# Optimization experiments

Measured on AMD Instinct MI355X. Metric: run time of the kernel, lower is better.

The kernel has to match this reference:

```python
import jax, jax.numpy as jnp
import numpy as np

N_NODES = 20000
N_EDGES = 320000
F_IN = 256
HID = 256
N_CLS = 5


def _glorot(key, shape):
    lim = np.sqrt(6.0 / (shape[0] + shape[1]))
    return jax.random.uniform(key, shape, jnp.float32, -lim, lim)


def setup_inputs() -> dict:
    key = jax.random.key(0)
    ks = jax.random.split(key, 12)
    x1 = jax.random.normal(ks[0], (N_NODES, F_IN), jnp.float32)
    x2 = jax.random.normal(ks[1], (N_NODES, F_IN), jnp.float32)
    ei1 = jax.random.randint(ks[2], (2, N_EDGES), 0, N_NODES, jnp.int64 if jax.config.jax_enable_x64 else jnp.int32)
    ei2 = jax.random.randint(ks[3], (2, N_EDGES), 0, N_NODES, jnp.int64 if jax.config.jax_enable_x64 else jnp.int32)
    params = {
        'W1': _glorot(ks[4], (F_IN, HID)), 'b1': jnp.zeros((HID,), jnp.float32),
        'W2': _glorot(ks[5], (HID, HID)), 'b2': jnp.zeros((HID,), jnp.float32),
        'W3': _glorot(ks[6], (HID, HID)), 'b3': jnp.zeros((HID,), jnp.float32),
        'Wl': _glorot(ks[7], (HID, N_CLS)), 'bl': jnp.zeros((N_CLS,), jnp.float32),
    }
    return {'x1': x1, 'edge_index1': ei1, 'x2': x2, 'edge_index2': ei2, **params}


def gcn_conv(x, edge_index, W, b):
    # PyG GCNConv: add self-loops, symmetric normalization D^-1/2 (A+I) D^-1/2 (X W) + b
    N = x.shape[0]
    src, dst = edge_index[0], edge_index[1]
    deg = jax.ops.segment_sum(jnp.ones(src.shape[0], x.dtype), dst, num_segments=N) + 1.0
    dinv = jax.lax.rsqrt(deg)  # [N]
    xw = x @ W                 # [N, H]
    coef = (dinv[src] * dinv[dst])[:, None]  # per-edge norm
    agg = jax.ops.segment_sum(xw[src] * coef, dst, num_segments=N)
    agg = agg + xw * (dinv * dinv)[:, None]  # self-loop term
    return agg + b


def _branch(x, ei, W1, b1, W2, b2, W3, b3):
    # dropout is identity in eval mode
    h = jax.nn.relu(gcn_conv(x, ei, W1, b1))
    h = jax.nn.relu(gcn_conv(h, ei, W2, b2))
    return gcn_conv(h, ei, W3, b3)


def reference(x1, edge_index1, x2, edge_index2, W1, b1, W2, b2, W3, b3, Wl, bl):
    h1 = _branch(x1, edge_index1, W1, b1, W2, b2, W3, b3)
    h2 = _branch(x2, edge_index2, W1, b1, W2, b2, W3, b3)
    h = jnp.concatenate([h1, h2], axis=0)          # [2N, H]
    pooled = jnp.mean(h, axis=0, keepdims=True)    # batch is all zeros -> single mean pool
    return pooled @ Wl + bl                        # [1, num_classes]
```

## Files before the change

### kernel.cpp

```cpp
#include <hip/hip_runtime.h>
#include <hip/hip_bf16.h>

#define N_NODES 20000
#define N_EDGES 320000
#define HID 256

typedef __attribute__((ext_vector_type(8))) short bf16x8;
typedef __attribute__((ext_vector_type(4))) float f32x4;

__device__ __forceinline__ float bf2f(ushort u) {
  union { unsigned int i; float f; } v; v.i = ((unsigned int)u) << 16; return v.f;
}
__device__ __forceinline__ ushort f2bf(float f) {
  union { float f; unsigned int i; } v; v.f = f;
  unsigned int r = v.i + 0x7FFFu + ((v.i >> 16) & 1u);
  return (ushort)(r >> 16);
}

__global__ void detect_kernel(const void* x1, const void* ei1, int* flags) {
  __shared__ int cnt_wild, cnt_oddnz;
  if (threadIdx.x == 0) { cnt_wild = 0; cnt_oddnz = 0; }
  __syncthreads();
  const ushort* xu = (const ushort*)x1;
  int wild = 0;
#pragma unroll
  for (int k = 0; k < 4; k++) {
    ushort u = xu[threadIdx.x * 4 + k];
    int ex = (u >> 7) & 0xFF;
    if (ex >= 0x90) wild++;
  }
  if (wild) atomicAdd(&cnt_wild, wild);
  const int* ii = (const int*)ei1;
  if (ii[threadIdx.x * 2 + 1] != 0) atomicAdd(&cnt_oddnz, 1);
  __syncthreads();
  if (threadIdx.x == 0) {
    flags[0] = (cnt_wild > 64) ? 1 : 0;
    flags[1] = (cnt_oddnz < 8) ? 1 : 0;
  }
}

__global__ void init_kernel(int* cnt0, int* cnt1, float* t0, float* t1) {
  int i = blockIdx.x * blockDim.x + threadIdx.x;
  if (i < N_NODES) { cnt0[i] = 0; cnt1[i] = 0; t0[i] = 0.f; t1[i] = 0.f; }
}

__global__ void cvt_ei_count_kernel(const void* e0, const void* e1,
                                    int* o0, int* o1,
                                    int* cnt0, int* cnt1,
                                    int* rank0, int* rank1, const int* flags) {
  int b = blockIdx.y;
  const void* e = b ? e1 : e0;
  int* o = b ? o1 : o0;
  int* cnt = b ? cnt1 : cnt0;
  int* rank = b ? rank1 : rank0;
  int i = blockIdx.x * 256 + threadIdx.x;
  if (i >= 2 * N_EDGES) return;
  int v = flags[1] ? (int)((const long long*)e)[i] : ((const int*)e)[i];
  o[i] = v;
  if (i >= N_EDGES) rank[i - N_EDGES] = atomicAdd(&cnt[v], 1);
}

__global__ void cvt_x_kernel(const void* x0, const void* x1v,
                             ushort* o0, ushort* o1, const int* flags) {
  const void* x = blockIdx.y ? x1v : x0;
  ushort* o = blockIdx.y ? o1 : o0;
  int i4 = (blockIdx.x * 256 + threadIdx.x) * 4;
  if (i4 >= N_NODES * HID) return;
  if (flags[0]) {
    float4 v = *(const float4*)((const float*)x + i4);
    ushort4 w; w.x = f2bf(v.x); w.y = f2bf(v.y); w.z = f2bf(v.z); w.w = f2bf(v.w);
    *(ushort4*)(o + i4) = w;
  } else {
    *(ushort4*)(o + i4) = *(const ushort4*)((const ushort*)x + i4);
  }
}

__global__ void cvt_w_kernel(const void* W1, const void* W2, const void* W3, const void* Wl,
                             const void* b1, const void* b2, const void* b3, const void* bl,
                             ushort* out, const int* flags) {
  int i = blockIdx.x * 256 + threadIdx.x;
  if (i >= 198661) return;
  const void* src; int off;
  if (i < 65536)       { src = W1; off = 0; }
  else if (i < 131072) { src = W2; off = 65536; }
  else if (i < 196608) { src = W3; off = 131072; }
  else if (i < 197888) { src = Wl; off = 196608; }
  else if (i < 198144) { src = b1; off = 197888; }
  else if (i < 198400) { src = b2; off = 198144; }
  else if (i < 198656) { src = b3; off = 198400; }
  else                 { src = bl; off = 198656; }
  int j = i - off;
  out[i] = flags[0] ? f2bf(((const float*)src)[j]) : ((const ushort*)src)[j];
}

__global__ __launch_bounds__(1024) void scan_kernel(const int* cnt0, const int* cnt1,
                                                    int* rp0, int* rp1,
                                                    float* dinv0, float* dinv1) {
  const int* cnt = blockIdx.x ? cnt1 : cnt0;
  int* rp = blockIdx.x ? rp1 : rp0;
  float* dinv = blockIdx.x ? dinv1 : dinv0;
  __shared__ int sd[1024];
  int tid = threadIdx.x;
  int base = tid * 20;
  int pref[20];
  int run = 0;
#pragma unroll
  for (int k = 0; k < 20; k++) {
    int i = base + k;
    int c = (i < N_NODES) ? cnt[i] : 0;
    if (i < N_NODES) dinv[i] = rsqrtf((float)c + 1.0f);
    run += c;
    pref[k] = run;
  }
  sd[tid] = run;
  __syncthreads();
  for (int off = 1; off < 1024; off <<= 1) {
    int v = (tid >= off) ? sd[tid - off] : 0;
    __syncthreads();
    sd[tid] += v;
    __syncthreads();
  }
  int offset = sd[tid] - run;
  if (tid == 0) rp[0] = 0;
#pragma unroll
  for (int k = 0; k < 20; k++) {
    int i = base + k;
    if (i < N_NODES) rp[i + 1] = offset + pref[k];
  }
}

__global__ void fill_kernel(const int* ei0, const int* ei1,
                            const float* dinv0, const float* dinv1,
                            const int* rp0, const int* rp1,
                            const int* rank0, const int* rank1,
                            int2* eg0, int2* eg1,
                            float* t0, float* t1) {
  int e = blockIdx.x * blockDim.x + threadIdx.x;
  if (e >= N_EDGES) return;
  int b = blockIdx.y;
  const int* ei = b ? ei1 : ei0;
  const float* dinv = b ? dinv1 : dinv0;
  const int* rp = b ? rp1 : rp0;
  const int* rank = b ? rank1 : rank0;
  int2* eg = b ? eg1 : eg0;
  float* t = b ? t1 : t0;
  int src = ei[e], dst = ei[N_EDGES + e];
  int slot = rp[dst] + rank[e];
  float dd = dinv[dst];
  eg[slot] = make_int2(src, __float_as_int(dinv[src] * dd));
  atomicAdd(&t[src], dd);
}

__global__ __launch_bounds__(256) void gemm_kernel(
    const ushort* __restrict__ A0, const ushort* __restrict__ A1,
    const ushort* __restrict__ W,
    ushort* __restrict__ C0, ushort* __restrict__ C1) {
  const ushort* A = blockIdx.z ? A1 : A0;
  ushort* C = blockIdx.z ? C1 : C0;
  int m0 = blockIdx.x * 64;
  int n0 = blockIdx.y * 64;
  __shared__ ushort As[64][40];
  __shared__ ushort Bs[64][40];
  int tid = threadIdx.x;
  int wave = tid >> 6, lane = tid & 63;
  int quad = lane >> 4, r16 = lane & 15;
  f32x4 acc0 = {0.f, 0.f, 0.f, 0.f}, acc1 = acc0, acc2 = acc0, acc3 = acc0;
  int la_row = tid >> 2;
  int la_off = (tid & 3) * 8;
  int lb_k = tid >> 3;
  int lb_n = (tid & 7) * 8;
  for (int k0 = 0; k0 < 256; k0 += 32) {
    int gr = m0 + la_row;
    int4 va = {0, 0, 0, 0};
    if (gr < N_NODES) va = *(const int4*)(A + gr * 256 + k0 + la_off);
    *(int4*)&As[la_row][la_off] = va;
    int4 vb = *(const int4*)(W + (k0 + lb_k) * 256 + n0 + lb_n);
    ushort tmp[8];
    *(int4*)tmp = vb;
#pragma unroll
    for (int j = 0; j < 8; j++) Bs[lb_n + j][lb_k] = tmp[j];
    __syncthreads();
    bf16x8 a  = *(const bf16x8*)&As[wave * 16 + r16][quad * 8];
    bf16x8 b0 = *(const bf16x8*)&Bs[r16][quad * 8];
    bf16x8 b1 = *(const bf16x8*)&Bs[16 + r16][quad * 8];
    bf16x8 b2 = *(const bf16x8*)&Bs[32 + r16][quad * 8];
    bf16x8 b3 = *(const bf16x8*)&Bs[48 + r16][quad * 8];
    acc0 = __builtin_amdgcn_mfma_f32_16x16x32_bf16(a, b0, acc0, 0, 0, 0);
    acc1 = __builtin_amdgcn_mfma_f32_16x16x32_bf16(a, b1, acc1, 0, 0, 0);
    acc2 = __builtin_amdgcn_mfma_f32_16x16x32_bf16(a, b2, acc2, 0, 0, 0);
    acc3 = __builtin_amdgcn_mfma_f32_16x16x32_bf16(a, b3, acc3, 0, 0, 0);
    __syncthreads();
  }
  int orow = m0 + wave * 16 + quad * 4;
#pragma unroll
  for (int r = 0; r < 4; r++) {
    int gr = orow + r;
    if (gr < N_NODES) {
      ushort* cp = C + gr * 256 + n0 + r16;
      cp[0]  = f2bf(acc0[r]);
      cp[16] = f2bf(acc1[r]);
      cp[32] = f2bf(acc2[r]);
      cp[48] = f2bf(acc3[r]);
    }
  }
}

__global__ __launch_bounds__(256) void agg_kernel(
    const ushort* __restrict__ XW0, const ushort* __restrict__ XW1,
    const float* __restrict__ dinv0, const float* __restrict__ dinv1,
    const int* __restrict__ rp0, const int* __restrict__ rp1,
    const int2* __restrict__ eg0, const int2* __restrict__ eg1,
    const ushort* __restrict__ bias,
    ushort* __restrict__ H0, ushort* __restrict__ H1) {
  int b = blockIdx.y;
  const ushort* XW = b ? XW1 : XW0;
  const float* dinv = b ? dinv1 : dinv0;
  const int* rp = b ? rp1 : rp0;
  const int2* eg = b ? eg1 : eg0;
  ushort* H = b ? H1 : H0;
  int wave = threadIdx.x >> 6, lane = threadIdx.x & 63;
  int i = blockIdx.x * 4 + wave;
  int f4 = lane * 4;
  float di = dinv[i];
  float self = di * di;
  ushort4 v = *(const ushort4*)(XW + i * 256 + f4);
  float a0 = self * bf2f(v.x), a1 = self * bf2f(v.y);
  float a2 = self * bf2f(v.z), a3 = self * bf2f(v.w);
  float c0_ = 0.f, c1_ = 0.f, c2_ = 0.f, c3_ = 0.f;
  int e0 = rp[i], e1 = rp[i + 1];
  int e = e0;
  for (; e + 3 < e1; e += 4) {
    int2 p0 = eg[e], p1 = eg[e + 1], p2 = eg[e + 2], p3 = eg[e + 3];
    ushort4 u0 = *(const ushort4*)(XW + p0.x * 256 + f4);
    ushort4 u1 = *(const ushort4*)(XW + p1.x * 256 + f4);
    ushort4 u2 = *(const ushort4*)(XW + p2.x * 256 + f4);
    ushort4 u3 = *(const ushort4*)(XW + p3.x * 256 + f4);
    float w0 = __int_as_float(p0.y), w1 = __int_as_float(p1.y);
    float w2 = __int_as_float(p2.y), w3 = __int_as_float(p3.y);
    a0 += w0 * bf2f(u0.x); a1 += w0 * bf2f(u0.y); a2 += w0 * bf2f(u0.z); a3 += w0 * bf2f(u0.w);
    c0_ += w1 * bf2f(u1.x); c1_ += w1 * bf2f(u1.y); c2_ += w1 * bf2f(u1.z); c3_ += w1 * bf2f(u1.w);
    a0 += w2 * bf2f(u2.x); a1 += w2 * bf2f(u2.y); a2 += w2 * bf2f(u2.z); a3 += w2 * bf2f(u2.w);
    c0_ += w3 * bf2f(u3.x); c1_ += w3 * bf2f(u3.y); c2_ += w3 * bf2f(u3.z); c3_ += w3 * bf2f(u3.w);
  }
  for (; e < e1; e++) {
    int2 pp = eg[e];
    float c = __int_as_float(pp.y);
    ushort4 u = *(const ushort4*)(XW + pp.x * 256 + f4);
    a0 += c * bf2f(u.x); a1 += c * bf2f(u.y); a2 += c * bf2f(u.z); a3 += c * bf2f(u.w);
  }
  a0 += c0_; a1 += c1_; a2 += c2_; a3 += c3_;
  ushort4 bb = *(const ushort4*)(bias + f4);
  a0 = fmaxf(a0 + bf2f(bb.x), 0.f);
  a1 = fmaxf(a1 + bf2f(bb.y), 0.f);
  a2 = fmaxf(a2 + bf2f(bb.z), 0.f);
  a3 = fmaxf(a3 + bf2f(bb.w), 0.f);
  ushort4 o; o.x = f2bf(a0); o.y = f2bf(a1); o.z = f2bf(a2); o.w = f2bf(a3);
  *(ushort4*)(H + i * 256 + f4) = o;
}

__global__ __launch_bounds__(256) void colsum_kernel(
    const ushort* __restrict__ H0, const ushort* __restrict__ H1,
    const float* __restrict__ dinv0, const float* __restrict__ dinv1,
    const float* __restrict__ t0, const float* __restrict__ t1,
    float* __restrict__ P) {
  int b = blockIdx.y;
  const ushort* H = b ? H1 : H0;
  const float* dinv = b ? dinv1 : dinv0;
  const float* t = b ? t1 : t0;
  int wave = threadIdx.x >> 6, lane = threadIdx.x & 63;
  int wid = blockIdx.x * 4 + wave;
  int f4 = lane * 4;
  float a0 = 0.f, a1 = 0.f, a2 = 0.f, a3 = 0.f;
  for (int j = wid; j < N_NODES; j += 256) {
    float dj = dinv[j];
    float c = dj * (t[j] + dj);
    ushort4 u = *(const ushort4*)(H + j * 256 + f4);
    a0 += c * bf2f(u.x); a1 += c * bf2f(u.y);
    a2 += c * bf2f(u.z); a3 += c * bf2f(u.w);
  }
  __shared__ float part[4][256];
  part[wave][f4 + 0] = a0; part[wave][f4 + 1] = a1;
  part[wave][f4 + 2] = a2; part[wave][f4 + 3] = a3;
  __syncthreads();
  int f = threadIdx.x;
  float ssum = part[0][f] + part[1][f] + part[2][f] + part[3][f];
  P[(b * 64 + blockIdx.x) * 256 + f] = ssum;
}

__global__ __launch_bounds__(256) void final_kernel(
    const float* __restrict__ P,
    const ushort* __restrict__ W3, const ushort* __restrict__ b3,
    const ushort* __restrict__ Wl, const ushort* __restrict__ bl,
    void* __restrict__ out, const int* __restrict__ flags) {
  __shared__ float v[256];
  __shared__ float pooled[256];
  int t = threadIdx.x;
  float acc0 = 0.f, acc1 = 0.f;
  for (int b = 0; b < 64; b++) {
    acc0 += P[b * 256 + t];
    acc1 += P[(64 + b) * 256 + t];
  }
  v[t] = acc0 + acc1;
  __syncthreads();
  float acc = 0.f;
  for (int f = 0; f < 256; f++) acc += v[f] * bf2f(W3[f * 256 + t]);
  pooled[t] = acc * (1.0f / (2.0f * N_NODES)) + bf2f(b3[t]);
  __syncthreads();
  if (t < 5) {
    float o = bf2f(bl[t]);
    for (int h = 0; h < 256; h++) o += pooled[h] * bf2f(Wl[h * 5 + t]);
    if (flags[0]) ((float*)out)[t] = o;
    else ((ushort*)out)[t] = f2bf(o);
  }
}

extern "C" void kernel_launch(void* const* d_in, const int* in_sizes, int n_in,
                              void* d_out, int out_size, void* d_ws, size_t ws_size,
                              hipStream_t stream) {
  const void* x1 = d_in[0];
  const void* ei1 = d_in[1];
  const void* x2 = d_in[2];
  const void* ei2 = d_in[3];
  const void* W1 = d_in[4];
  const void* b1 = d_in[5];
  const void* W2 = d_in[6];
  const void* b2 = d_in[7];
  const void* W3 = d_in[8];
  const void* b3 = d_in[9];
  const void* Wl = d_in[10];
  const void* bl = d_in[11];

  char* p = (char*)d_ws;
  auto alloc = [&](size_t bytes) {
    char* r = p;
    p += (bytes + 255) & ~size_t(255);
    return r;
  };
  int* flags   = (int*)alloc(256);
  float* dinv0 = (float*)alloc(N_NODES * 4);
  float* dinv1 = (float*)alloc(N_NODES * 4);
  float* t0    = (float*)alloc(N_NODES * 4);
  float* t1    = (float*)alloc(N_NODES * 4);
  int* cnt0    = (int*)alloc(N_NODES * 4);
  int* cnt1    = (int*)alloc(N_NODES * 4);
  int* rp0     = (int*)alloc((N_NODES + 1) * 4);
  int* rp1     = (int*)alloc((N_NODES + 1) * 4);
  int2* eg0    = (int2*)alloc((size_t)N_EDGES * 8);
  int2* eg1    = (int2*)alloc((size_t)N_EDGES * 8);
  float* Pp    = (float*)alloc(2 * 64 * 256 * 4);
  ushort* wbuf = (ushort*)alloc(198661 * 2);
  ushort* xw0  = (ushort*)alloc((size_t)N_NODES * HID * 2);
  ushort* xw1  = (ushort*)alloc((size_t)N_NODES * HID * 2);
  ushort* xc0  = (ushort*)alloc((size_t)N_NODES * HID * 2);
  ushort* xc1  = (ushort*)alloc((size_t)N_NODES * HID * 2);
  int* ei32_0 = (int*)xw0;
  int* ei32_1 = ei32_0 + 2 * N_EDGES;
  int* rank0  = ei32_1 + 2 * N_EDGES;
  int* rank1  = rank0 + N_EDGES;
  ushort* h0 = xc0;
  ushort* h1 = xc1;

  ushort* Wc1 = wbuf + 0;
  ushort* Wc2 = wbuf + 65536;
  ushort* Wc3 = wbuf + 131072;
  ushort* Wlc = wbuf + 196608;
  ushort* bc1 = wbuf + 197888;
  ushort* bc2 = wbuf + 198144;
  ushort* bc3 = wbuf + 198400;
  ushort* blc = wbuf + 198656;

  detect_kernel<<<1, 256, 0, stream>>>(x1, ei1, flags);
  init_kernel<<<(N_NODES + 255) / 256, 256, 0, stream>>>(cnt0, cnt1, t0, t1);
  cvt_ei_count_kernel<<<dim3((2 * N_EDGES + 255) / 256, 2), 256, 0, stream>>>(
      ei1, ei2, ei32_0, ei32_1, cnt0, cnt1, rank0, rank1, flags);
  cvt_x_kernel<<<dim3(N_NODES * HID / 1024, 2), 256, 0, stream>>>(
      x1, x2, xc0, xc1, flags);
  cvt_w_kernel<<<(198661 + 255) / 256, 256, 0, stream>>>(
      W1, W2, W3, Wl, b1, b2, b3, bl, wbuf, flags);
  scan_kernel<<<2, 1024, 0, stream>>>(cnt0, cnt1, rp0, rp1, dinv0, dinv1);
  fill_kernel<<<dim3((N_EDGES + 255) / 256, 2), 256, 0, stream>>>(
      ei32_0, ei32_1, dinv0, dinv1, rp0, rp1, rank0, rank1, eg0, eg1, t0, t1);

  gemm_kernel<<<dim3(313, 4, 2), 256, 0, stream>>>(xc0, xc1, Wc1, xw0, xw1);
  agg_kernel<<<dim3(N_NODES / 4, 2), 256, 0, stream>>>(
      xw0, xw1, dinv0, dinv1, rp0, rp1, eg0, eg1, bc1, h0, h1);

  gemm_kernel<<<dim3(313, 4, 2), 256, 0, stream>>>(h0, h1, Wc2, xw0, xw1);
  agg_kernel<<<dim3(N_NODES / 4, 2), 256, 0, stream>>>(
      xw0, xw1, dinv0, dinv1, rp0, rp1, eg0, eg1, bc2, h0, h1);

  colsum_kernel<<<dim3(64, 2), 256, 0, stream>>>(h0, h1, dinv0, dinv1, t0, t1, Pp);
  final_kernel<<<1, 256, 0, stream>>>(Pp, Wc3, bc3, Wlc, blc, d_out, flags);
}
```

Measured before the change: 414.5 us.

## Pre-transpose W1/W2 for vectorized GEMM loads; split aggregation wave into half-wave edge streams

The weight conversion kernel now stores W1 and W2 transposed, so the GEMM can load the B tile with 16-byte vector stores instead of scattering eight scalar LDS writes per thread. The aggregation kernel now has each half-wave handle alternate edges with 16-byte gathers of 8 features per lane, combining halves with a cross-lane shuffle before bias, ReLU and store. This aims to raise gather width and memory-level parallelism in the edge aggregation, at the cost of a shuffle and half the lanes idle on the store. W3 is not transposed, so any GEMM call that uses W3 would read it in the wrong layout.

Result: faster. 381.4 us (-8.0%).

```diff
diff --git a/kernel.cpp b/kernel.cpp
--- a/kernel.cpp
+++ b/kernel.cpp
@@ -7,6 +7,7 @@
 
 typedef __attribute__((ext_vector_type(8))) short bf16x8;
 typedef __attribute__((ext_vector_type(4))) float f32x4;
+typedef __attribute__((ext_vector_type(8))) unsigned short us8;
 
 __device__ __forceinline__ float bf2f(ushort u) {
   union { unsigned int i; float f; } v; v.i = ((unsigned int)u) << 16; return v.f;
@@ -80,9 +81,9 @@
                              ushort* out, const int* flags) {
   int i = blockIdx.x * 256 + threadIdx.x;
   if (i >= 198661) return;
-  const void* src; int off;
-  if (i < 65536)       { src = W1; off = 0; }
-  else if (i < 131072) { src = W2; off = 65536; }
+  const void* src; int off; bool tr = false;
+  if (i < 65536)       { src = W1; off = 0; tr = true; }
+  else if (i < 131072) { src = W2; off = 65536; tr = true; }
   else if (i < 196608) { src = W3; off = 131072; }
   else if (i < 197888) { src = Wl; off = 196608; }
   else if (i < 198144) { src = b1; off = 197888; }
@@ -90,6 +91,7 @@
   else if (i < 198656) { src = b3; off = 198400; }
   else                 { src = bl; off = 198656; }
   int j = i - off;
+  if (tr) j = (j & 255) * 256 + (j >> 8);
   out[i] = flags[0] ? f2bf(((const float*)src)[j]) : ((const ushort*)src)[j];
 }
 
@@ -153,7 +155,7 @@
 
 __global__ __launch_bounds__(256) void gemm_kernel(
     const ushort* __restrict__ A0, const ushort* __restrict__ A1,
-    const ushort* __restrict__ W,
+    const ushort* __restrict__ Wt,
     ushort* __restrict__ C0, ushort* __restrict__ C1) {
   const ushort* A = blockIdx.z ? A1 : A0;
   ushort* C = blockIdx.z ? C1 : C0;
@@ -165,20 +167,15 @@
   int wave = tid >> 6, lane = tid & 63;
   int quad = lane >> 4, r16 = lane & 15;
   f32x4 acc0 = {0.f, 0.f, 0.f, 0.f}, acc1 = acc0, acc2 = acc0, acc3 = acc0;
-  int la_row = tid >> 2;
-  int la_off = (tid & 3) * 8;
-  int lb_k = tid >> 3;
-  int lb_n = (tid & 7) * 8;
+  int l_row = tid >> 2;
+  int l_off = (tid & 3) * 8;
   for (int k0 = 0; k0 < 256; k0 += 32) {
-    int gr = m0 + la_row;
+    int gr = m0 + l_row;
     int4 va = {0, 0, 0, 0};
-    if (gr < N_NODES) va = *(const int4*)(A + gr * 256 + k0 + la_off);
-    *(int4*)&As[la_row][la_off] = va;
-    int4 vb = *(const int4*)(W + (k0 + lb_k) * 256 + n0 + lb_n);
-    ushort tmp[8];
-    *(int4*)tmp = vb;
-#pragma unroll
-    for (int j = 0; j < 8; j++) Bs[lb_n + j][lb_k] = tmp[j];
+    if (gr < N_NODES) va = *(const int4*)(A + gr * 256 + k0 + l_off);
+    *(int4*)&As[l_row][l_off] = va;
+    int4 vb = *(const int4*)(Wt + (n0 + l_row) * 256 + k0 + l_off);
+    *(int4*)&Bs[l_row][l_off] = vb;
     __syncthreads();
     bf16x8 a  = *(const bf16x8*)&As[wave * 16 + r16][quad * 8];
     bf16x8 b0 = *(const bf16x8*)&Bs[r16][quad * 8];
@@ -219,43 +216,62 @@
   const int2* eg = b ? eg1 : eg0;
   ushort* H = b ? H1 : H0;
   int wave = threadIdx.x >> 6, lane = threadIdx.x & 63;
+  int half = lane >> 5;
+  int fl = (lane & 31) * 8;
   int i = blockIdx.x * 4 + wave;
-  int f4 = lane * 4;
   float di = dinv[i];
-  float self = di * di;
-  ushort4 v = *(const ushort4*)(XW + i * 256 + f4);
-  float a0 = self * bf2f(v.x), a1 = self * bf2f(v.y);
-  float a2 = self * bf2f(v.z), a3 = self * bf2f(v.w);
-  float c0_ = 0.f, c1_ = 0.f, c2_ = 0.f, c3_ = 0.f;
+  float selfw = half ? 0.f : di * di;
+  us8 v = *(const us8*)(XW + i * 256 + fl);
+  float accA[8], accB[8];
+#pragma unroll
+  for (int j = 0; j < 8; j++) { accA[j] = selfw * bf2f(v[j]); accB[j] = 0.f; }
   int e0 = rp[i], e1 = rp[i + 1];
-  int e = e0;
-  for (; e + 3 < e1; e += 4) {
-    int2 p0 = eg[e], p1 = eg[e + 1], p2 = eg[e + 2], p3 = eg[e + 3];
-    ushort4 u0 = *(const ushort4*)(XW + p0.x * 256 + f4);
-    ushort4 u1 = *(const ushort4*)(XW + p1.x * 256 + f4);
-    ushort4 u2 = *(const ushort4*)(XW + p2.x * 256 + f4);
-    ushort4 u3 = *(const ushort4*)(XW + p3.x * 256 + f4);
+  int n = e1 - e0;
+  int npair = n >> 1;
+  int pe = 0;
+  for (; pe + 3 < npair; pe += 4) {
+    int ea = e0 + 2 * pe + half;
+    int2 p0 = eg[ea];
+    int2 p1 = eg[ea + 2];
+    int2 p2 = eg[ea + 4];
+    int2 p3 = eg[ea + 6];
+    us8 r0 = *(const us8*)(XW + p0.x * 256 + fl);
+    us8 r1 = *(const us8*)(XW + p1.x * 256 + fl);
+    us8 r2 = *(const us8*)(XW + p2.x * 256 + fl);
+    us8 r3 = *(const us8*)(XW + p3.x * 256 + fl);
     float w0 = __int_as_float(p0.y), w1 = __int_as_float(p1.y);
     float w2 = __int_as_float(p2.y), w3 = __int_as_float(p3.y);
-    a0 += w0 * bf2f(u0.x); a1 += w0 * bf2f(u0.y); a2 += w0 * bf2f(u0.z); a3 += w0 * bf2f(u0.w);
-    c0_ += w1 * bf2f(u1.x); c1_ += w1 * bf2f(u1.y); c2_ += w1 * bf2f(u1.z); c3_ += w1 * bf2f(u1.w);
-    a0 += w2 * bf2f(u2.x); a1 += w2 * bf2f(u2.y); a2 += w2 * bf2f(u2.z); a3 += w2 * bf2f(u2.w);
-    c0_ += w3 * bf2f(u3.x); c1_ += w3 * bf2f(u3.y); c2_ += w3 * bf2f(u3.z); c3_ += w3 * bf2f(u3.w);
-  }
-  for (; e < e1; e++) {
-    int2 pp = eg[e];
-    float c = __int_as_float(pp.y);
-    ushort4 u = *(const ushort4*)(XW + pp.x * 256 + f4);
-    a0 += c * bf2f(u.x); a1 += c * bf2f(u.y); a2 += c * bf2f(u.z); a3 += c * bf2f(u.w);
-  }
-  a0 += c0_; a1 += c1_; a2 += c2_; a3 += c3_;
-  ushort4 bb = *(const ushort4*)(bias + f4);
-  a0 = fmaxf(a0 + bf2f(bb.x), 0.f);
-  a1 = fmaxf(a1 + bf2f(bb.y), 0.f);
-  a2 = fmaxf(a2 + bf2f(bb.z), 0.f);
-  a3 = fmaxf(a3 + bf2f(bb.w), 0.f);
-  ushort4 o; o.x = f2bf(a0); o.y = f2bf(a1); o.z = f2bf(a2); o.w = f2bf(a3);
-  *(ushort4*)(H + i * 256 + f4) = o;
+#pragma unroll
+    for (int j = 0; j < 8; j++) {
+      accA[j] += w0 * bf2f(r0[j]);
+      accB[j] += w1 * bf2f(r1[j]);
+      accA[j] += w2 * bf2f(r2[j]);
+      accB[j] += w3 * bf2f(r3[j]);
+    }
+  }
+  for (; pe < npair; pe++) {
+    int2 pp = eg[e0 + 2 * pe + half];
+    us8 r = *(const us8*)(XW + pp.x * 256 + fl);
+    float w = __int_as_float(pp.y);
+#pragma unroll
+    for (int j = 0; j < 8; j++) accA[j] += w * bf2f(r[j]);
+  }
+  if (n & 1) {
+    int2 pp = eg[e1 - 1];
+    float w = half ? 0.f : __int_as_float(pp.y);
+    us8 r = *(const us8*)(XW + pp.x * 256 + fl);
+#pragma unroll
+    for (int j = 0; j < 8; j++) accB[j] += w * bf2f(r[j]);
+  }
+  us8 bb = *(const us8*)(bias + fl);
+  us8 o;
+#pragma unroll
+  for (int j = 0; j < 8; j++) {
+    float s = accA[j] + accB[j];
+    s += __shfl_xor(s, 32);
+    o[j] = f2bf(fmaxf(s + bf2f(bb[j]), 0.f));
+  }
+  if (half == 0) *(us8*)(H + i * 256 + fl) = o;
 }
 
 __global__ __launch_bounds__(256) void colsum_kernel(
```
